# Kernel tuning notes

Hardware: AMD Instinct MI355X
Metric: run time of the kernel (lower is better)

The kernel has to match this reference:

```python
import jax, jax.numpy as jnp
import numpy as np

B, S, D = 8, 1024, 768
H = 12
DH = D // H  # 64


def setup_inputs() -> dict:
    key = jax.random.key(0)
    ks = jax.random.split(key, 9)
    s = 0.02
    return {
        "x": jax.random.normal(ks[0], (B, S, D), dtype=jnp.float32),
        # per-head QKV projections stacked over heads: [H, D, DH]
        "Wq": jax.random.normal(ks[1], (H, D, DH), dtype=jnp.float32) * s,
        "bq": jax.random.normal(ks[2], (H, DH), dtype=jnp.float32) * s,
        "Wk": jax.random.normal(ks[3], (H, D, DH), dtype=jnp.float32) * s,
        "bk": jax.random.normal(ks[4], (H, DH), dtype=jnp.float32) * s,
        "Wv": jax.random.normal(ks[5], (H, D, DH), dtype=jnp.float32) * s,
        "bv": jax.random.normal(ks[6], (H, DH), dtype=jnp.float32) * s,
        # output projection: [D, D] (applied as x @ Wo + bo)
        "Wo": jax.random.normal(ks[7], (D, D), dtype=jnp.float32) * s,
        "bo": jax.random.normal(ks[8], (D,), dtype=jnp.float32) * s,
    }


def reference(x, Wq, bq, Wk, bk, Wv, bv, Wo, bo):
    # Per-head linear projections, vectorized over heads -> [B, H, S, DH]
    q = jnp.einsum("bsd,hde->bhse", x, Wq) + bq[None, :, None, :]
    k = jnp.einsum("bsd,hde->bhse", x, Wk) + bk[None, :, None, :]
    v = jnp.einsum("bsd,hde->bhse", x, Wv) + bv[None, :, None, :]
    scale = 1.0 / jnp.sqrt(jnp.asarray(DH, dtype=q.dtype))
    scores = jnp.einsum("bhse,bhte->bhst", q, k) * scale  # [B,H,S,S]
    probs = jax.nn.softmax(scores, axis=-1)  # dropout p=0 (eval)
    out = jnp.einsum("bhst,bhte->bhse", probs, v)  # [B,H,S,DH]
    # concat heads (head order matches ModuleList order) -> [B,S,D]
    out = out.transpose(0, 2, 1, 3).reshape(B, S, D)
    return out @ Wo + bo
```

## Files before the change

kernel.cpp:

```cpp
#include <hip/hip_runtime.h>
#include <math.h>

#define BB 8
#define SS 1024
#define DD 768
#define HH 12
#define DHH 64
#define BSS (BB*SS)

typedef _Float16 half8 __attribute__((ext_vector_type(8)));
typedef _Float16 half4 __attribute__((ext_vector_type(4)));
typedef float    f32x4 __attribute__((ext_vector_type(4)));

__global__ __launch_bounds__(256)
void cast_x_f16(const float* __restrict__ x, _Float16* __restrict__ xh)
{
    int i = blockIdx.x * 256 + threadIdx.x;
    float4 v = ((const float4*)x)[i];
    half4 h = { (_Float16)v.x, (_Float16)v.y, (_Float16)v.z, (_Float16)v.w };
    ((half4*)xh)[i] = h;
}

__device__ __forceinline__
void transpose_tile(const float* __restrict__ src, _Float16* __restrict__ dst,
                    int d0, int n_outer, int base_mul, int row_stride, int tid)
{
    __shared__ float T[64][65];
    const size_t base = (size_t)n_outer * base_mul;
    {
        int dl = tid >> 2, c0 = (tid & 3) * 16;
        const float* p = src + base + (size_t)(d0 + dl) * row_stride + c0;
#pragma unroll
        for (int m = 0; m < 4; ++m) {
            float4 f = *(const float4*)(p + m * 4);
            T[dl][c0 + m*4 + 0] = f.x;
            T[dl][c0 + m*4 + 1] = f.y;
            T[dl][c0 + m*4 + 2] = f.z;
            T[dl][c0 + m*4 + 3] = f.w;
        }
    }
    __syncthreads();
    {
        int e = tid >> 2, c = tid & 3;
        half8 lo, hi;
#pragma unroll
        for (int i = 0; i < 8; ++i) {
            lo[i] = (_Float16)T[c*16 + i][e];
            hi[i] = (_Float16)T[c*16 + 8 + i][e];
        }
        _Float16* q = dst + ((size_t)n_outer * 64 + e) * DD + d0 + c * 16;
        *(half8*)q = lo;
        *(half8*)(q + 8) = hi;
    }
}

__global__ __launch_bounds__(256)
void transpose_qkv_w(const float* __restrict__ Wq, const float* __restrict__ Wk,
                     const float* __restrict__ Wv,
                     _Float16* __restrict__ Wqt, _Float16* __restrict__ Wkt,
                     _Float16* __restrict__ Wvt)
{
    const float* src = (blockIdx.z == 0) ? Wq : (blockIdx.z == 1) ? Wk : Wv;
    _Float16*   dst  = (blockIdx.z == 0) ? Wqt : (blockIdx.z == 1) ? Wkt : Wvt;
    transpose_tile(src, dst, blockIdx.x * 64, blockIdx.y, DD * DHH, DHH, threadIdx.x);
}

__global__ __launch_bounds__(256)
void transpose_wo(const float* __restrict__ Wo, _Float16* __restrict__ Wot)
{
    transpose_tile(Wo, Wot, blockIdx.x * 64, blockIdx.y, 64, DD, threadIdx.x);
}

__global__ __launch_bounds__(256)
void gemm_qkv_fused(const _Float16* __restrict__ Ah,
                    const _Float16* __restrict__ Bq, const _Float16* __restrict__ Bk,
                    const _Float16* __restrict__ Bv,
                    const float* __restrict__ bqv, const float* __restrict__ bkv,
                    const float* __restrict__ bvv,
                    _Float16* __restrict__ oq, _Float16* __restrict__ ok,
                    _Float16* __restrict__ ov)
{
    __shared__ _Float16 Ash[128][40];
    __shared__ _Float16 Bsh[3][64][40];

    const int tid  = threadIdx.x;
    const int wave = tid >> 6;
    const int lane = tid & 15;
    const int quad = (tid >> 4) & 3;
    const int m0 = blockIdx.x * 128;
    const int n0 = blockIdx.y * 64;

    const _Float16* Bt[3] = { Bq, Bk, Bv };

    f32x4 acc[3][2][4];
#pragma unroll
    for (int w = 0; w < 3; ++w)
#pragma unroll
        for (int i = 0; i < 2; ++i)
#pragma unroll
            for (int j = 0; j < 4; ++j) acc[w][i][j] = (f32x4){0.f, 0.f, 0.f, 0.f};

    for (int k0 = 0; k0 < DD; k0 += 32) {
        __syncthreads();
#pragma unroll
        for (int c = 0; c < 2; ++c) {
            int chunk = tid + c * 256;
            int r = chunk >> 2, hf = chunk & 3;
            *(half8*)&Ash[r][hf * 8] =
                *(const half8*)(Ah + (size_t)(m0 + r) * DD + k0 + hf * 8);
        }
        {
            int r = tid >> 2, hf = tid & 3;
#pragma unroll
            for (int w = 0; w < 3; ++w)
                *(half8*)&Bsh[w][r][hf * 8] =
                    *(const half8*)(Bt[w] + (size_t)(n0 + r) * DD + k0 + hf * 8);
        }
        __syncthreads();

        half8 a[2];
#pragma unroll
        for (int i = 0; i < 2; ++i)
            a[i] = *(const half8*)&Ash[wave * 32 + i * 16 + lane][quad * 8];
#pragma unroll
        for (int w = 0; w < 3; ++w) {
#pragma unroll
            for (int j = 0; j < 4; ++j) {
                half8 b = *(const half8*)&Bsh[w][j * 16 + lane][quad * 8];
#pragma unroll
                for (int i = 0; i < 2; ++i)
                    acc[w][i][j] = __builtin_amdgcn_mfma_f32_16x16x32_f16(a[i], b, acc[w][i][j], 0, 0, 0);
            }
        }
    }

    const float* bias[3] = { bqv, bkv, bvv };
    _Float16*    dst[3]  = { oq, ok, ov };
#pragma unroll
    for (int w = 0; w < 3; ++w) {
#pragma unroll
        for (int i = 0; i < 2; ++i) {
#pragma unroll
            for (int r = 0; r < 4; ++r) {
                int row = m0 + wave * 32 + i * 16 + quad * 4 + r;
                int b = row >> 10;
                int s = row & (SS - 1);
#pragma unroll
                for (int j = 0; j < 4; ++j) {
                    int col = n0 + j * 16 + lane;
                    int h = col >> 6, e = col & 63;
                    float vv = acc[w][i][j][r] + bias[w][col];
                    dst[w][((size_t)(b * HH + h) * SS + s) * DHH + e] = (_Float16)vv;
                }
            }
        }
    }
}

__global__ __launch_bounds__(256)
void gemm_out_f16(const _Float16* __restrict__ Ah, const _Float16* __restrict__ Bt,
                  const float* __restrict__ bias, float* __restrict__ out)
{
    __shared__ _Float16 Ash[128][40];
    __shared__ _Float16 Bsh[64][40];
    const int tid  = threadIdx.x;
    const int wave = tid >> 6;
    const int lane = tid & 15;
    const int quad = (tid >> 4) & 3;
    const int m0 = blockIdx.x * 128;
    const int n0 = blockIdx.y * 64;

    f32x4 acc[2][4];
#pragma unroll
    for (int i = 0; i < 2; ++i)
#pragma unroll
        for (int j = 0; j < 4; ++j) acc[i][j] = (f32x4){0.f, 0.f, 0.f, 0.f};

    for (int k0 = 0; k0 < DD; k0 += 32) {
        __syncthreads();
#pragma unroll
        for (int c = 0; c < 2; ++c) {
            int chunk = tid + c * 256;
            int r = chunk >> 2, hf = chunk & 3;
            *(half8*)&Ash[r][hf * 8] =
                *(const half8*)(Ah + (size_t)(m0 + r) * DD + k0 + hf * 8);
        }
        {
            int r = tid >> 2, hf = tid & 3;
            *(half8*)&Bsh[r][hf * 8] =
                *(const half8*)(Bt + (size_t)(n0 + r) * DD + k0 + hf * 8);
        }
        __syncthreads();

        half8 a[2], b[4];
#pragma unroll
        for (int i = 0; i < 2; ++i)
            a[i] = *(const half8*)&Ash[wave * 32 + i * 16 + lane][quad * 8];
#pragma unroll
        for (int j = 0; j < 4; ++j)
            b[j] = *(const half8*)&Bsh[j * 16 + lane][quad * 8];
#pragma unroll
        for (int i = 0; i < 2; ++i)
#pragma unroll
            for (int j = 0; j < 4; ++j)
                acc[i][j] = __builtin_amdgcn_mfma_f32_16x16x32_f16(a[i], b[j], acc[i][j], 0, 0, 0);
    }

#pragma unroll
    for (int i = 0; i < 2; ++i) {
#pragma unroll
        for (int r = 0; r < 4; ++r) {
            int row = m0 + wave * 32 + i * 16 + quad * 4 + r;
#pragma unroll
            for (int j = 0; j < 4; ++j) {
                int col = n0 + j * 16 + lane;
                out[(size_t)row * DD + col] = acc[i][j][r] + bias[col];
            }
        }
    }
}

__global__ __launch_bounds__(256)
void vtrans(const _Float16* __restrict__ v, _Float16* __restrict__ vt)
{
    __shared__ _Float16 T[64][66];
    const int bh = blockIdx.x;
    const int s0 = blockIdx.y * 64;
    const int tid = threadIdx.x;

    const _Float16* vb = v + ((size_t)bh * SS + s0) * DHH;
    {
        int r = tid >> 2, c0 = (tid & 3) * 16;
        *(half8*)&T[r][c0]     = *(const half8*)(vb + (size_t)r * DHH + c0);
        *(half8*)&T[r][c0 + 8] = *(const half8*)(vb + (size_t)r * DHH + c0 + 8);
    }
    __syncthreads();
    {
        int e = tid >> 2, c = tid & 3;
        half8 lo, hi;
#pragma unroll
        for (int i = 0; i < 8; ++i) {
            lo[i] = T[c*16 + i][e];
            hi[i] = T[c*16 + 8 + i][e];
        }
        _Float16* q = vt + ((size_t)bh * DHH + e) * SS + s0 + c * 16;
        *(half8*)q = lo;
        *(half8*)(q + 8) = hi;
    }
}

__global__ __launch_bounds__(256)
void attn_f16(const _Float16* __restrict__ qh, const _Float16* __restrict__ kh,
              const _Float16* __restrict__ vt, _Float16* __restrict__ ctxh)
{
    const int bh  = blockIdx.x;
    const int q0  = blockIdx.y * 64;
    const int tid = threadIdx.x;
    const int wave = tid >> 6;
    const int lane = tid & 15;
    const int quad = (tid >> 4) & 3;

    __shared__ _Float16 Qs[64][72];
    __shared__ _Float16 Ks[64][72];
    __shared__ _Float16 Vt[64][72];
    __shared__ _Float16 Pf[4][16][72];

    const _Float16* qb  = qh + ((size_t)bh * SS + q0) * DHH;
    const _Float16* kb  = kh + (size_t)bh * SS * DHH;
    const _Float16* vtb = vt + (size_t)bh * DHH * SS;

    {
        int r = tid >> 2, c0 = (tid & 3) * 16;
        half8 q1 = *(const half8*)(qb + (size_t)r * DHH + c0);
        half8 q2 = *(const half8*)(qb + (size_t)r * DHH + c0 + 8);
        q1 = q1 * (_Float16)0.125f;
        q2 = q2 * (_Float16)0.125f;
        *(half8*)&Qs[r][c0]     = q1;
        *(half8*)&Qs[r][c0 + 8] = q2;
    }
    __syncthreads();

    const half8 qlo = *(const half8*)&Qs[wave * 16 + lane][quad * 8];
    const half8 qhi = *(const half8*)&Qs[wave * 16 + lane][32 + quad * 8];

    f32x4 o[4];
    float lacc[4];
#pragma unroll
    for (int j = 0; j < 4; ++j) o[j] = (f32x4){0.f, 0.f, 0.f, 0.f};
#pragma unroll
    for (int r = 0; r < 4; ++r) lacc[r] = 0.f;

    for (int kt = 0; kt < SS; kt += 64) {
        __syncthreads();
        {
            int r = tid >> 2, c0 = (tid & 3) * 16;
            *(half8*)&Ks[r][c0]     = *(const half8*)(kb + (size_t)(kt + r) * DHH + c0);
            *(half8*)&Ks[r][c0 + 8] = *(const half8*)(kb + (size_t)(kt + r) * DHH + c0 + 8);
            *(half8*)&Vt[r][c0]     = *(const half8*)(vtb + (size_t)r * SS + kt + c0);
            *(half8*)&Vt[r][c0 + 8] = *(const half8*)(vtb + (size_t)r * SS + kt + c0 + 8);
        }
        __syncthreads();

#pragma unroll
        for (int f = 0; f < 4; ++f) {
            half8 klo = *(const half8*)&Ks[f * 16 + lane][quad * 8];
            half8 khi = *(const half8*)&Ks[f * 16 + lane][32 + quad * 8];
            f32x4 z = (f32x4){0.f, 0.f, 0.f, 0.f};
            z = __builtin_amdgcn_mfma_f32_16x16x32_f16(qlo, klo, z, 0, 0, 0);
            z = __builtin_amdgcn_mfma_f32_16x16x32_f16(qhi, khi, z, 0, 0, 0);
#pragma unroll
            for (int r = 0; r < 4; ++r) {
                float p = __expf(z[r]);
                lacc[r] += p;
                Pf[wave][quad * 4 + r][f * 16 + lane] = (_Float16)p;
            }
        }

        half8 pl = *(const half8*)&Pf[wave][lane][quad * 8];
        half8 ph = *(const half8*)&Pf[wave][lane][32 + quad * 8];

#pragma unroll
        for (int j = 0; j < 4; ++j) {
            half8 vlo = *(const half8*)&Vt[j * 16 + lane][quad * 8];
            half8 vhi = *(const half8*)&Vt[j * 16 + lane][32 + quad * 8];
            o[j] = __builtin_amdgcn_mfma_f32_16x16x32_f16(pl, vlo, o[j], 0, 0, 0);
            o[j] = __builtin_amdgcn_mfma_f32_16x16x32_f16(ph, vhi, o[j], 0, 0, 0);
        }
    }

    const int b_ = bh / HH;
    const int h_ = bh % HH;
#pragma unroll
    for (int r = 0; r < 4; ++r) {
        float lr = lacc[r];
#pragma unroll
        for (int msk = 1; msk < 16; msk <<= 1)
            lr += __shfl_xor(lr, msk, 16);
        float invl = 1.f / lr;
        int s_ = q0 + wave * 16 + quad * 4 + r;
        _Float16* orow = ctxh + ((size_t)(b_ * SS + s_)) * DD + h_ * DHH;
#pragma unroll
        for (int j = 0; j < 4; ++j)
            orow[j * 16 + lane] = (_Float16)(o[j][r] * invl);
    }
}

extern "C" void kernel_launch(void* const* d_in, const int* in_sizes, int n_in,
                              void* d_out, int out_size, void* d_ws, size_t ws_size,
                              hipStream_t stream)
{
    const float* x  = (const float*)d_in[0];
    const float* Wq = (const float*)d_in[1];
    const float* bq = (const float*)d_in[2];
    const float* Wk = (const float*)d_in[3];
    const float* bk = (const float*)d_in[4];
    const float* Wv = (const float*)d_in[5];
    const float* bv = (const float*)d_in[6];
    const float* Wo = (const float*)d_in[7];
    const float* bo = (const float*)d_in[8];
    float* out = (float*)d_out;

    const size_t xe = (size_t)BSS * DD;
    const size_t we = (size_t)DD * DD;
    _Float16* Xh   = (_Float16*)d_ws;
    _Float16* Wqt  = Xh  + xe;
    _Float16* Wkt  = Wqt + we;
    _Float16* Wvt  = Wkt + we;
    _Float16* Wot  = Wvt + we;
    _Float16* qhb  = Wot + we;
    _Float16* khb  = qhb + xe;
    _Float16* vhb  = khb + xe;
    _Float16* vtb  = vhb + xe;
    _Float16* ctxh = vtb + xe;

    cast_x_f16<<<xe / 4 / 256, 256, 0, stream>>>(x, Xh);

    dim3 tg3(DD / 64, DD / 64, 3);
    transpose_qkv_w<<<tg3, 256, 0, stream>>>(Wq, Wk, Wv, Wqt, Wkt, Wvt);
    dim3 tg(DD / 64, DD / 64);
    transpose_wo<<<tg, 256, 0, stream>>>(Wo, Wot);

    dim3 gg(BSS / 128, DD / 64);
    gemm_qkv_fused<<<gg, 256, 0, stream>>>(Xh, Wqt, Wkt, Wvt, bq, bk, bv,
                                           qhb, khb, vhb);

    dim3 vg(BB * HH, SS / 64);
    vtrans<<<vg, 256, 0, stream>>>(vhb, vtb);

    attn_f16<<<vg, 256, 0, stream>>>(qhb, khb, vtb, ctxh);

    gemm_out_f16<<<gg, 256, 0, stream>>>(ctxh, Wot, bo, out);
}
```

Before: 251.5 us.

## Fuse x cast and V transpose into stacked 128x128 QKV GEMM, merge weight transposes

Removes the separate x-to-f16 cast kernel by converting fp32 x to half while loading the GEMM A tile, and treats Q/K/V weights as one stacked 2304-wide matrix processed with 128x128 tiles and a grouped block-index swizzle. The V output is written directly in transposed layout, which eliminates the vtrans kernel, and the four weight transposes become one launch. The attention kernel swaps the MFMA operands so P is produced already transposed, which allows packed half4 stores and a single row-sum reduction. The trade-offs are strided scattered stores for V^T, repeated fp32 reads and conversion of x across the N tiles, and higher register use from 16 accumulators per wave.

```diff
diff --git a/kernel.cpp b/kernel.cpp
--- a/kernel.cpp
+++ b/kernel.cpp
@@ -7,19 +7,11 @@
 #define HH 12
 #define DHH 64
 #define BSS (BB*SS)
+#define NQKV 2304
 
 typedef _Float16 half8 __attribute__((ext_vector_type(8)));
 typedef _Float16 half4 __attribute__((ext_vector_type(4)));
 typedef float    f32x4 __attribute__((ext_vector_type(4)));
-
-__global__ __launch_bounds__(256)
-void cast_x_f16(const float* __restrict__ x, _Float16* __restrict__ xh)
-{
-    int i = blockIdx.x * 256 + threadIdx.x;
-    float4 v = ((const float4*)x)[i];
-    half4 h = { (_Float16)v.x, (_Float16)v.y, (_Float16)v.z, (_Float16)v.w };
-    ((half4*)xh)[i] = h;
-}
 
 __device__ __forceinline__
 void transpose_tile(const float* __restrict__ src, _Float16* __restrict__ dst,
@@ -55,103 +47,118 @@
 }
 
 __global__ __launch_bounds__(256)
-void transpose_qkv_w(const float* __restrict__ Wq, const float* __restrict__ Wk,
-                     const float* __restrict__ Wv,
-                     _Float16* __restrict__ Wqt, _Float16* __restrict__ Wkt,
-                     _Float16* __restrict__ Wvt)
-{
-    const float* src = (blockIdx.z == 0) ? Wq : (blockIdx.z == 1) ? Wk : Wv;
-    _Float16*   dst  = (blockIdx.z == 0) ? Wqt : (blockIdx.z == 1) ? Wkt : Wvt;
-    transpose_tile(src, dst, blockIdx.x * 64, blockIdx.y, DD * DHH, DHH, threadIdx.x);
+void transpose_all(const float* __restrict__ Wq, const float* __restrict__ Wk,
+                   const float* __restrict__ Wv, const float* __restrict__ Wo,
+                   _Float16* __restrict__ Wt, _Float16* __restrict__ Wot)
+{
+    const int z = blockIdx.z;
+    const float* src;
+    _Float16* dst;
+    int base_mul, row_stride;
+    if (z < 3) {
+        src = (z == 0) ? Wq : (z == 1) ? Wk : Wv;
+        dst = Wt + (size_t)z * DD * DD;
+        base_mul = DD * DHH; row_stride = DHH;
+    } else {
+        src = Wo; dst = Wot;
+        base_mul = 64; row_stride = DD;
+    }
+    transpose_tile(src, dst, blockIdx.x * 64, blockIdx.y, base_mul, row_stride,
+                   threadIdx.x);
 }
 
 __global__ __launch_bounds__(256)
-void transpose_wo(const float* __restrict__ Wo, _Float16* __restrict__ Wot)
-{
-    transpose_tile(Wo, Wot, blockIdx.x * 64, blockIdx.y, 64, DD, threadIdx.x);
-}
-
-__global__ __launch_bounds__(256)
-void gemm_qkv_fused(const _Float16* __restrict__ Ah,
-                    const _Float16* __restrict__ Bq, const _Float16* __restrict__ Bk,
-                    const _Float16* __restrict__ Bv,
-                    const float* __restrict__ bqv, const float* __restrict__ bkv,
-                    const float* __restrict__ bvv,
-                    _Float16* __restrict__ oq, _Float16* __restrict__ ok,
-                    _Float16* __restrict__ ov)
+void gemm_qkv_stacked(const float* __restrict__ X, const _Float16* __restrict__ Wt,
+                      const float* __restrict__ bq, const float* __restrict__ bk,
+                      const float* __restrict__ bv,
+                      _Float16* __restrict__ qo, _Float16* __restrict__ ko,
+                      _Float16* __restrict__ vto)
 {
     __shared__ _Float16 Ash[128][40];
-    __shared__ _Float16 Bsh[3][64][40];
+    __shared__ _Float16 Bsh[128][40];
+
+    const int b = blockIdx.x;
+    const int c  = b & 7;
+    const int g  = b >> 3;
+    const int n_t = g % 18;
+    const int m_t = (g / 18) * 8 + c;
+    const int m0 = m_t * 128;
+    const int n0 = n_t * 128;
 
     const int tid  = threadIdx.x;
     const int wave = tid >> 6;
     const int lane = tid & 15;
     const int quad = (tid >> 4) & 3;
-    const int m0 = blockIdx.x * 128;
-    const int n0 = blockIdx.y * 64;
-
-    const _Float16* Bt[3] = { Bq, Bk, Bv };
-
-    f32x4 acc[3][2][4];
-#pragma unroll
-    for (int w = 0; w < 3; ++w)
-#pragma unroll
-        for (int i = 0; i < 2; ++i)
-#pragma unroll
-            for (int j = 0; j < 4; ++j) acc[w][i][j] = (f32x4){0.f, 0.f, 0.f, 0.f};
+    const int wy = wave >> 1;
+    const int wx = wave & 1;
+
+    f32x4 acc[4][4];
+#pragma unroll
+    for (int i = 0; i < 4; ++i)
+#pragma unroll
+        for (int j = 0; j < 4; ++j) acc[i][j] = (f32x4){0.f, 0.f, 0.f, 0.f};
+
+    const int st_row = 0;
+    (void)st_row;
 
     for (int k0 = 0; k0 < DD; k0 += 32) {
         __syncthreads();
 #pragma unroll
-        for (int c = 0; c < 2; ++c) {
-            int chunk = tid + c * 256;
-            int r = chunk >> 2, hf = chunk & 3;
-            *(half8*)&Ash[r][hf * 8] =
-                *(const half8*)(Ah + (size_t)(m0 + r) * DD + k0 + hf * 8);
-        }
-        {
-            int r = tid >> 2, hf = tid & 3;
-#pragma unroll
-            for (int w = 0; w < 3; ++w)
-                *(half8*)&Bsh[w][r][hf * 8] =
-                    *(const half8*)(Bt[w] + (size_t)(n0 + r) * DD + k0 + hf * 8);
-        }
-        __syncthreads();
-
-        half8 a[2];
-#pragma unroll
-        for (int i = 0; i < 2; ++i)
-            a[i] = *(const half8*)&Ash[wave * 32 + i * 16 + lane][quad * 8];
-#pragma unroll
-        for (int w = 0; w < 3; ++w) {
+        for (int cc = 0; cc < 2; ++cc) {
+            int chunk = tid + cc * 256;
+            int row = chunk >> 2, col8 = chunk & 3;
+            const float* src = X + (size_t)(m0 + row) * DD + k0 + col8 * 8;
+            float4 u = *(const float4*)src;
+            float4 u2 = *(const float4*)(src + 4);
+            half8 hv = { (_Float16)u.x, (_Float16)u.y, (_Float16)u.z, (_Float16)u.w,
+                         (_Float16)u2.x, (_Float16)u2.y, (_Float16)u2.z, (_Float16)u2.w };
+            *(half8*)&Ash[row][col8 * 8] = hv;
+        }
+#pragma unroll
+        for (int cc = 0; cc < 2; ++cc) {
+            int chunk = tid + cc * 256;
+            int row = chunk >> 2, col8 = chunk & 3;
+            *(half8*)&Bsh[row][col8 * 8] =
+                *(const half8*)(Wt + (size_t)(n0 + row) * DD + k0 + col8 * 8);
+        }
+        __syncthreads();
+
+        half8 a[4], bf[4];
+#pragma unroll
+        for (int i = 0; i < 4; ++i)
+            a[i] = *(const half8*)&Ash[wy * 64 + i * 16 + lane][quad * 8];
+#pragma unroll
+        for (int j = 0; j < 4; ++j)
+            bf[j] = *(const half8*)&Bsh[wx * 64 + j * 16 + lane][quad * 8];
+#pragma unroll
+        for (int i = 0; i < 4; ++i)
+#pragma unroll
+            for (int j = 0; j < 4; ++j)
+                acc[i][j] = __builtin_amdgcn_mfma_f32_16x16x32_f16(a[i], bf[j], acc[i][j], 0, 0, 0);
+    }
+
+    const int w = n0 / 768;
+    const float* bp = (w == 0) ? bq : (w == 1) ? bk : bv;
+    const int nb = n0 - w * 768 + wx * 64;
+
+#pragma unroll
+    for (int i = 0; i < 4; ++i) {
+#pragma unroll
+        for (int r = 0; r < 4; ++r) {
+            int row = m0 + wy * 64 + i * 16 + quad * 4 + r;
+            int b_ = row >> 10;
+            int s  = row & (SS - 1);
 #pragma unroll
             for (int j = 0; j < 4; ++j) {
-                half8 b = *(const half8*)&Bsh[w][j * 16 + lane][quad * 8];
-#pragma unroll
-                for (int i = 0; i < 2; ++i)
-                    acc[w][i][j] = __builtin_amdgcn_mfma_f32_16x16x32_f16(a[i], b, acc[w][i][j], 0, 0, 0);
-            }
-        }
-    }
-
-    const float* bias[3] = { bqv, bkv, bvv };
-    _Float16*    dst[3]  = { oq, ok, ov };
-#pragma unroll
-    for (int w = 0; w < 3; ++w) {
-#pragma unroll
-        for (int i = 0; i < 2; ++i) {
-#pragma unroll
-            for (int r = 0; r < 4; ++r) {
-                int row = m0 + wave * 32 + i * 16 + quad * 4 + r;
-                int b = row >> 10;
-                int s = row & (SS - 1);
-#pragma unroll
-                for (int j = 0; j < 4; ++j) {
-                    int col = n0 + j * 16 + lane;
-                    int h = col >> 6, e = col & 63;
-                    float vv = acc[w][i][j][r] + bias[w][col];
-                    dst[w][((size_t)(b * HH + h) * SS + s) * DHH + e] = (_Float16)vv;
-                }
+                int nl = nb + j * 16 + lane;
+                int h = nl >> 6, e = nl & 63;
+                float val = acc[i][j][r] + bp[nl];
+                if (w == 0)
+                    qo[((size_t)(b_ * HH + h) * SS + s) * DHH + e] = (_Float16)val;
+                else if (w == 1)
+                    ko[((size_t)(b_ * HH + h) * SS + s) * DHH + e] = (_Float16)val;
+                else
+                    vto[((size_t)(b_ * HH + h) * DHH + e) * SS + s] = (_Float16)val;
             }
         }
     }
@@ -179,8 +186,8 @@
     for (int k0 = 0; k0 < DD; k0 += 32) {
         __syncthreads();
 #pragma unroll
-        for (int c = 0; c < 2; ++c) {
-            int chunk = tid + c * 256;
+        for (int cc = 0; cc < 2; ++cc) {
+            int chunk = tid + cc * 256;
             int r = chunk >> 2, hf = chunk & 3;
             *(half8*)&Ash[r][hf * 8] =
                 *(const half8*)(Ah + (size_t)(m0 + r) * DD + k0 + hf * 8);
@@ -192,18 +199,18 @@
         }
         __syncthreads();
 
-        half8 a[2], b[4];
+        half8 a[2], bfr[4];
 #pragma unroll
         for (int i = 0; i < 2; ++i)
             a[i] = *(const half8*)&Ash[wave * 32 + i * 16 + lane][quad * 8];
 #pragma unroll
         for (int j = 0; j < 4; ++j)
-            b[j] = *(const half8*)&Bsh[j * 16 + lane][quad * 8];
+            bfr[j] = *(const half8*)&Bsh[j * 16 + lane][quad * 8];
 #pragma unroll
         for (int i = 0; i < 2; ++i)
 #pragma unroll
             for (int j = 0; j < 4; ++j)
-                acc[i][j] = __builtin_amdgcn_mfma_f32_16x16x32_f16(a[i], b[j], acc[i][j], 0, 0, 0);
+                acc[i][j] = __builtin_amdgcn_mfma_f32_16x16x32_f16(a[i], bfr[j], acc[i][j], 0, 0, 0);
     }
 
 #pragma unroll
@@ -217,35 +224,6 @@
                 out[(size_t)row * DD + col] = acc[i][j][r] + bias[col];
             }
         }
-    }
-}
-
-__global__ __launch_bounds__(256)
-void vtrans(const _Float16* __restrict__ v, _Float16* __restrict__ vt)
-{
-    __shared__ _Float16 T[64][66];
-    const int bh = blockIdx.x;
-    const int s0 = blockIdx.y * 64;
-    const int tid = threadIdx.x;
-
-    const _Float16* vb = v + ((size_t)bh * SS + s0) * DHH;
-    {
-        int r = tid >> 2, c0 = (tid & 3) * 16;
-        *(half8*)&T[r][c0]     = *(const half8*)(vb + (size_t)r * DHH + c0);
-        *(half8*)&T[r][c0 + 8] = *(const half8*)(vb + (size_t)r * DHH + c0 + 8);
-    }
-    __syncthreads();
-    {
-        int e = tid >> 2, c = tid & 3;
-        half8 lo, hi;
-#pragma unroll
-        for (int i = 0; i < 8; ++i) {
-            lo[i] = T[c*16 + i][e];
-            hi[i] = T[c*16 + 8 + i][e];
-        }
-        _Float16* q = vt + ((size_t)bh * DHH + e) * SS + s0 + c * 16;
-        *(half8*)q = lo;
-        *(half8*)(q + 8) = hi;
     }
 }
 
@@ -263,7 +241,7 @@
     __shared__ _Float16 Qs[64][72];
     __shared__ _Float16 Ks[64][72];
     __shared__ _Float16 Vt[64][72];
-    __shared__ _Float16 Pf[4][16][72];
+    __shared__ _Float16 Pt[4][16][72];
 
     const _Float16* qb  = qh + ((size_t)bh * SS + q0) * DHH;
     const _Float16* kb  = kh + (size_t)bh * SS * DHH;
@@ -284,11 +262,9 @@
     const half8 qhi = *(const half8*)&Qs[wave * 16 + lane][32 + quad * 8];
 
     f32x4 o[4];
-    float lacc[4];
+    float lacc = 0.f;
 #pragma unroll
     for (int j = 0; j < 4; ++j) o[j] = (f32x4){0.f, 0.f, 0.f, 0.f};
-#pragma unroll
-    for (int r = 0; r < 4; ++r) lacc[r] = 0.f;
 
     for (int kt = 0; kt < SS; kt += 64) {
         __syncthreads();
@@ -306,18 +282,20 @@
             half8 klo = *(const half8*)&Ks[f * 16 + lane][quad * 8];
             half8 khi = *(const half8*)&Ks[f * 16 + lane][32 + quad * 8];
             f32x4 z = (f32x4){0.f, 0.f, 0.f, 0.f};
-            z = __builtin_amdgcn_mfma_f32_16x16x32_f16(qlo, klo, z, 0, 0, 0);
-            z = __builtin_amdgcn_mfma_f32_16x16x32_f16(qhi, khi, z, 0, 0, 0);
+            z = __builtin_amdgcn_mfma_f32_16x16x32_f16(klo, qlo, z, 0, 0, 0);
+            z = __builtin_amdgcn_mfma_f32_16x16x32_f16(khi, qhi, z, 0, 0, 0);
+            half4 pk;
 #pragma unroll
             for (int r = 0; r < 4; ++r) {
                 float p = __expf(z[r]);
-                lacc[r] += p;
-                Pf[wave][quad * 4 + r][f * 16 + lane] = (_Float16)p;
+                lacc += p;
+                pk[r] = (_Float16)p;
             }
-        }
-
-        half8 pl = *(const half8*)&Pf[wave][lane][quad * 8];
-        half8 ph = *(const half8*)&Pf[wave][lane][32 + quad * 8];
+            *(half4*)&Pt[wave][lane][f * 16 + quad * 4] = pk;
+        }
+
+        half8 pl = *(const half8*)&Pt[wave][lane][quad * 8];
+        half8 ph = *(const half8*)&Pt[wave][lane][32 + quad * 8];
 
 #pragma unroll
         for (int j = 0; j < 4; ++j) {
@@ -328,15 +306,15 @@
         }
     }
 
+    float lr = lacc;
+    lr += __shfl_xor(lr, 16);
+    lr += __shfl_xor(lr, 32);
+
     const int b_ = bh / HH;
     const int h_ = bh % HH;
 #pragma unroll
     for (int r = 0; r < 4; ++r) {
-        float lr = lacc[r];
-#pragma unroll
-        for (int msk = 1; msk < 16; msk <<= 1)
-            lr += __shfl_xor(lr, msk, 16);
-        float invl = 1.f / lr;
+        float invl = 1.f / __shfl(lr, quad * 4 + r, 16);
         int s_ = q0 + wave * 16 + quad * 4 + r;
         _Float16* orow = ctxh + ((size_t)(b_ * SS + s_)) * DD + h_ * DHH;
 #pragma unroll
@@ -362,32 +340,22 @@
 
     const size_t xe = (size_t)BSS * DD;
     const size_t we = (size_t)DD * DD;
-    _Float16* Xh   = (_Float16*)d_ws;
-    _Float16* Wqt  = Xh  + xe;
-    _Float16* Wkt  = Wqt + we;
-    _Float16* Wvt  = Wkt + we;
-    _Float16* Wot  = Wvt + we;
+    _Float16* Wt   = (_Float16*)d_ws;
+    _Float16* Wot  = Wt  + (size_t)3 * we;
     _Float16* qhb  = Wot + we;
     _Float16* khb  = qhb + xe;
-    _Float16* vhb  = khb + xe;
-    _Float16* vtb  = vhb + xe;
+    _Float16* vtb  = khb + xe;
     _Float16* ctxh = vtb + xe;
 
-    cast_x_f16<<<xe / 4 / 256, 256, 0, stream>>>(x, Xh);
-
-    dim3 tg3(DD / 64, DD / 64, 3);
-    transpose_qkv_w<<<tg3, 256, 0, stream>>>(Wq, Wk, Wv, Wqt, Wkt, Wvt);
-    dim3 tg(DD / 64, DD / 64);
-    transpose_wo<<<tg, 256, 0, stream>>>(Wo, Wot);
+    dim3 tg(DD / 64, DD / 64, 4);
+    transpose_all<<<tg, 256, 0, stream>>>(Wq, Wk, Wv, Wo, Wt, Wot);
+
+    gemm_qkv_stacked<<<(BSS / 128) * (NQKV / 128), 256, 0, stream>>>(
+        x, Wt, bq, bk, bv, qhb, khb, vtb);
+
+    dim3 ag(BB * HH, SS / 64);
+    attn_f16<<<ag, 256, 0, stream>>>(qhb, khb, vtb, ctxh);
 
     dim3 gg(BSS / 128, DD / 64);
-    gemm_qkv_fused<<<gg, 256, 0, stream>>>(Xh, Wqt, Wkt, Wvt, bq, bk, bv,
-                                           qhb, khb, vhb);
-
-    dim3 vg(BB * HH, SS / 64);
-    vtrans<<<vg, 256, 0, stream>>>(vhb, vtb);
-
-    attn_f16<<<vg, 256, 0, stream>>>(qhb, khb, vtb, ctxh);
-
     gemm_out_f16<<<gg, 256, 0, stream>>>(ctxh, Wot, bo, out);
 }
```

Result: faster. 237.1 us (-5.7%).
